# Optimization experiments

Hardware: AMD Instinct MI355X
Metric: run time of the kernel (lower is better)

Reference implementation:

```python
import jax, jax.numpy as jnp
import numpy as np

SHAPES = ((100, 100), (50, 50), (25, 25))  # (H_l, W_l) per level
D, HEADS, HD, L, P = 256, 8, 32, 3, 4


def setup_inputs() -> dict:
    key = jax.random.key(0)
    ks = jax.random.split(key, 12)
    B = 2
    Nq = sum(h * w for h, w in SHAPES)  # 13125
    inp = {
        "query": jax.random.normal(ks[0], (B, Nq, D), jnp.float32),
        "reference_points": jax.random.uniform(ks[1], (B, Nq, L, 2), jnp.float32),
        "value0": jax.random.normal(ks[2], (B, SHAPES[0][0] * SHAPES[0][1], D), jnp.float32),
        "value1": jax.random.normal(ks[3], (B, SHAPES[1][0] * SHAPES[1][1], D), jnp.float32),
        "value2": jax.random.normal(ks[4], (B, SHAPES[2][0] * SHAPES[2][1], D), jnp.float32),
        "W_val": jax.random.normal(ks[5], (D, D), jnp.float32) * 0.05,
        "b_val": jnp.zeros((D,), jnp.float32),
        "W_off": jax.random.normal(ks[6], (D, HEADS * L * P * 2), jnp.float32) * 0.01,
        "b_off": jax.random.normal(ks[7], (HEADS * L * P * 2,), jnp.float32) * 2.0,
        "W_attn": jax.random.normal(ks[8], (D, HEADS * L * P), jnp.float32) * 0.02,
        "b_attn": jnp.zeros((HEADS * L * P,), jnp.float32),
        "W_out": jax.random.normal(ks[9], (D, D), jnp.float32) * 0.05,
        "b_out": jnp.zeros((D,), jnp.float32),
    }
    return inp


def _bilinear_sample(v, Hl, Wl, loc):
    """v: (B, heads, Hl*Wl, hd); loc: (B, Nq, heads, P, 2) normalized coords in [0,1].
    Matches torch F.grid_sample(mode='bilinear', padding_mode='zeros', align_corners=False)
    applied to grid = 2*loc - 1. Returns (B, Nq, heads, P, hd)."""
    B, heads, _, hd = v.shape
    Nq, Pn = loc.shape[1], loc.shape[3]
    # align_corners=False: pixel = ((g+1)*size - 1)/2 with g = 2*loc-1  ->  loc*size - 0.5
    x = loc[..., 0] * Wl - 0.5
    y = loc[..., 1] * Hl - 0.5
    x0 = jnp.floor(x)
    y0 = jnp.floor(y)
    wx1 = x - x0
    wy1 = y - y0
    out = jnp.zeros((B, Nq, heads, Pn, hd), v.dtype)
    for xi, wx in ((x0, 1.0 - wx1), (x0 + 1.0, wx1)):
        for yi, wy in ((y0, 1.0 - wy1), (y0 + 1.0, wy1)):
            inb = (xi >= 0) & (xi < Wl) & (yi >= 0) & (yi < Hl)
            idx = (jnp.clip(yi, 0, Hl - 1) * Wl + jnp.clip(xi, 0, Wl - 1)).astype(jnp.int32)
            idx_t = idx.transpose(0, 2, 1, 3).reshape(B, heads, Nq * Pn)  # (B,H,Nq*P)
            g = jnp.take_along_axis(v, idx_t[..., None], axis=2)  # (B,H,Nq*P,hd)
            g = g.reshape(B, heads, Nq, Pn, hd).transpose(0, 2, 1, 3, 4)
            w = (wx * wy * inb).astype(v.dtype)  # (B,Nq,heads,P)
            out = out + g * w[..., None]
    return out


def _forward(query, reference_points, values, W_val, b_val, W_off, b_off, W_attn, b_attn, W_out, b_out):
    B, Nq, _ = query.shape
    offs = (query @ W_off + b_off).reshape(B, Nq, HEADS, L, P, 2)
    attn = jax.nn.softmax((query @ W_attn + b_attn).reshape(B, Nq, HEADS, L * P), axis=-1)
    attn = attn.reshape(B, Nq, HEADS, L, P)
    out = jnp.zeros((B, Nq, HEADS, HD), query.dtype)
    for lvl, (Hl, Wl) in enumerate(SHAPES):
        # project values, split heads: (B, heads, H*W, hd)
        v = (values[lvl] @ W_val + b_val).reshape(B, Hl * Wl, HEADS, HD).transpose(0, 2, 1, 3)
        norm = jnp.array([Wl, Hl], query.dtype)
        loc = reference_points[:, :, lvl][:, :, None, None, :] + offs[:, :, :, lvl] / norm  # (B,Nq,heads,P,2)
        sampled = _bilinear_sample(v, Hl, Wl, loc)  # (B,Nq,heads,P,hd)
        out = out + jnp.einsum('bnhp,bnhpd->bnhd', attn[:, :, :, lvl], sampled)
    out = out.reshape(B, Nq, D)
    return out @ W_out + b_out  # dropout is identity at eval


def reference(query, reference_points, value0, value1, value2, W_val, b_val, W_off, b_off, W_attn, b_attn, W_out, b_out):
    return _forward(query, reference_points, (value0, value1, value2), W_val, b_val, W_off, b_off, W_attn, b_attn, W_out, b_out)
```

## Files before the change

### kernel.cpp

```cpp
#include <hip/hip_runtime.h>
#include <hip/hip_bf16.h>
#include <math.h>

#define BATCH 2
#define NQ    13125
#define MQ    26250
#define DM    256
#define NH    8
#define HDIM  32
#define NL    3
#define NP    4
#define NTOK  13125

typedef __attribute__((ext_vector_type(8))) short bf16x8;
typedef __attribute__((ext_vector_type(4))) float f32x4;
typedef __attribute__((ext_vector_type(2))) float f32x2;

__device__ __forceinline__ short f2bf(float f) {
    unsigned u = __float_as_uint(f);
    unsigned r = (u + 0x7FFFu + ((u >> 16) & 1u)) >> 16;
    return (short)r;
}
__device__ __forceinline__ float bf2f(unsigned short u) {
    return __uint_as_float((unsigned)u << 16);
}
__device__ __forceinline__ unsigned cvt_pk_bf16(float lo, float hi) {
    unsigned r;
    asm("v_cvt_pk_bf16_f32 %0, %1, %2" : "=v"(r) : "v"(lo), "v"(hi));
    return r;
}

__device__ __forceinline__ void gld_lds16(const short* g, short* l) {
    __builtin_amdgcn_global_load_lds(
        (const __attribute__((address_space(1))) unsigned int*)g,
        (__attribute__((address_space(3))) unsigned int*)l, 16, 0, 0);
}

__global__ __launch_bounds__(256) void wprep_kernel(const float* __restrict__ Wv,
                                                    const float* __restrict__ Wo,
                                                    const float* __restrict__ Wa,
                                                    const float* __restrict__ Wu,
                                                    short* __restrict__ Wt)
{
    const int bid = blockIdx.x;
    const int w  = bid >> 8;
    const int Ns[5]   = {256, 192, 96, 256, 96};
    const int Offs[5] = {0, 65536, 114688, 163840, 139264};
    const int N = Ns[w];
    const int flat = (bid & 255) * 256 + threadIdx.x;
    const int n = flat >> 8, k = flat & 255;
    if (n >= N) return;
    if (w == 4) { Wt[139264 + n * 256 + k] = 0; return; }
    const float* W = (w == 0) ? Wv : ((w == 1) ? Wo : ((w == 2) ? Wa : Wu));
    Wt[Offs[w] + n * 256 + k] = f2bf(W[k * N + n]);
}

__global__ __launch_bounds__(256) void gemm5_kernel(const float* __restrict__ query,
                                                    const float* __restrict__ v0,
                                                    const float* __restrict__ v1,
                                                    const float* __restrict__ v2,
                                                    const short* __restrict__ Wt_val,
                                                    const short* __restrict__ Wt_off,
                                                    const float* __restrict__ b_val,
                                                    const float* __restrict__ b_off,
                                                    const float* __restrict__ b_attn,
                                                    short* __restrict__ vws,
                                                    float* __restrict__ offs,
                                                    float* __restrict__ lgts)
{
    const int e = (blockIdx.x & 7) * 129 + (blockIdx.x >> 3);
    if (e >= 1030) return;
    const int y  = e % 5;
    const int m0 = (e / 5) * 128;

    __shared__ short As[128 * 32];
    __shared__ short Bs[128 * 32];

    const int tid  = threadIdx.x;
    const bool isv = (y < 2);
    const short* Wt = isv ? Wt_val : Wt_off;
    const int n0 = isv ? y * 128 : (y - 2) * 128;

    const int r  = tid >> 1;
    const int h  = tid & 1;
    const int gm = m0 + r;
    const int gmc = (gm < MQ) ? gm : (MQ - 1);
    const float* Arow;
    if (isv) {
        const int b  = gmc / NTOK;
        const int rr = gmc % NTOK;
        if (rr < 10000)      Arow = v0 + (size_t)(b * 10000 + rr) * 256;
        else if (rr < 12500) Arow = v1 + (size_t)(b * 2500 + rr - 10000) * 256;
        else                 Arow = v2 + (size_t)(b * 625 + rr - 12500) * 256;
    } else {
        Arow = query + (size_t)gmc * 256;
    }
    const int pA0 = ((h * 2 + 0) ^ ((r >> 1) & 3)) << 3;
    const int pA1 = ((h * 2 + 1) ^ ((r >> 1) & 3)) << 3;
    short* lAr = As + r * 32;

    const int row0 = tid >> 2;
    const int row1 = row0 + 64;
    const int kqs  = (tid & 3) ^ ((row0 >> 1) & 3);
    const short* gB0 = Wt + (size_t)(n0 + row0) * 256 + kqs * 8;
    const short* gB1 = Wt + (size_t)(n0 + row1) * 256 + kqs * 8;
    short* lB0 = Bs + tid * 8;
    short* lB1 = Bs + (256 + tid) * 8;

    const int lane = tid & 63;
    const int wave = tid >> 6;
    const int wm   = (wave & 1) * 64;
    const int wn   = (wave >> 1) * 64;
    const int ml   = lane & 15;
    const int kq   = lane >> 4;

    f32x4 acc[4][4] = {};

    for (int k0 = 0; k0 < 256; k0 += 32) {
        gld_lds16(gB0 + k0, lB0);
        gld_lds16(gB1 + k0, lB1);

        const float4 a0 = *(const float4*)(Arow + k0 + h * 16 + 0);
        const float4 a1 = *(const float4*)(Arow + k0 + h * 16 + 4);
        const float4 a2 = *(const float4*)(Arow + k0 + h * 16 + 8);
        const float4 a3 = *(const float4*)(Arow + k0 + h * 16 + 12);
        union { bf16x8 v; unsigned u[4]; } t0, t1;
        t0.u[0] = cvt_pk_bf16(a0.x, a0.y); t0.u[1] = cvt_pk_bf16(a0.z, a0.w);
        t0.u[2] = cvt_pk_bf16(a1.x, a1.y); t0.u[3] = cvt_pk_bf16(a1.z, a1.w);
        t1.u[0] = cvt_pk_bf16(a2.x, a2.y); t1.u[1] = cvt_pk_bf16(a2.z, a2.w);
        t1.u[2] = cvt_pk_bf16(a3.x, a3.y); t1.u[3] = cvt_pk_bf16(a3.z, a3.w);
        *(bf16x8*)(lAr + pA0) = t0.v;
        *(bf16x8*)(lAr + pA1) = t1.v;

        __syncthreads();

        bf16x8 af[4], bfr[4];
#pragma unroll
        for (int ti = 0; ti < 4; ++ti) {
            const int rr = wm + ti * 16 + ml;
            af[ti] = *(const bf16x8*)&As[rr * 32 + ((kq ^ ((rr >> 1) & 3)) << 3)];
        }
#pragma unroll
        for (int tj = 0; tj < 4; ++tj) {
            const int rr = wn + tj * 16 + ml;
            bfr[tj] = *(const bf16x8*)&Bs[rr * 32 + ((kq ^ ((rr >> 1) & 3)) << 3)];
        }
#pragma unroll
        for (int ti = 0; ti < 4; ++ti)
#pragma unroll
            for (int tj = 0; tj < 4; ++tj)
                acc[ti][tj] = __builtin_amdgcn_mfma_f32_16x16x32_bf16(af[ti], bfr[tj], acc[ti][tj], 0, 0, 0);

        __syncthreads();
    }

#pragma unroll
    for (int tj = 0; tj < 4; ++tj) {
        const int gn = n0 + wn + tj * 16 + ml;
#pragma unroll
        for (int ti = 0; ti < 4; ++ti) {
#pragma unroll
            for (int rr = 0; rr < 4; ++rr) {
                const int gmo = m0 + wm + ti * 16 + kq * 4 + rr;
                if (gmo >= MQ) continue;
                const float v = acc[ti][tj][rr];
                if (isv) {
                    vws[(size_t)gmo * 256 + gn] = f2bf(v + b_val[gn]);
                } else {
                    if (gn < 192)      offs[(size_t)gmo * 192 + gn]        = v + b_off[gn];
                    else if (gn < 288) lgts[(size_t)gmo * 96 + (gn - 192)] = v + b_attn[gn - 192];
                }
            }
        }
    }
}

__device__ __forceinline__ void gemm_core128(const short* __restrict__ A,
                                             const short* __restrict__ Wt,
                                             int m0, int n0,
                                             f32x4 (&acc)[4][4],
                                             short* As, short* Bs)
{
    const int tid  = threadIdx.x;
    const int lane = tid & 63;
    const int wave = tid >> 6;
    const int wm   = (wave & 1) * 64;
    const int wn   = (wave >> 1) * 64;
    const int ml   = lane & 15;
    const int kq   = lane >> 4;

    const int row0 = tid >> 2;
    const int row1 = row0 + 64;
    const int kqs  = (tid & 3) ^ ((row0 >> 1) & 3);
    const short* gA0 = A  + (size_t)(m0 + row0) * 256 + kqs * 8;
    const short* gA1 = A  + (size_t)(m0 + row1) * 256 + kqs * 8;
    const short* gB0 = Wt + (size_t)(n0 + row0) * 256 + kqs * 8;
    const short* gB1 = Wt + (size_t)(n0 + row1) * 256 + kqs * 8;
    short* lA0 = As + tid * 8;
    short* lA1 = As + (256 + tid) * 8;
    short* lB0 = Bs + tid * 8;
    short* lB1 = Bs + (256 + tid) * 8;
    const bool a0ok = (m0 + row0) < MQ;
    const bool a1ok = (m0 + row1) < MQ;

    for (int k0 = 0; k0 < 256; k0 += 32) {
        if (a0ok) gld_lds16(gA0 + k0, lA0);
        if (a1ok) gld_lds16(gA1 + k0, lA1);
        gld_lds16(gB0 + k0, lB0);
        gld_lds16(gB1 + k0, lB1);
        __syncthreads();

        bf16x8 af[4], bfr[4];
#pragma unroll
        for (int ti = 0; ti < 4; ++ti) {
            const int r = wm + ti * 16 + ml;
            af[ti] = *(const bf16x8*)&As[r * 32 + ((kq ^ ((r >> 1) & 3)) << 3)];
        }
#pragma unroll
        for (int tj = 0; tj < 4; ++tj) {
            const int r = wn + tj * 16 + ml;
            bfr[tj] = *(const bf16x8*)&Bs[r * 32 + ((kq ^ ((r >> 1) & 3)) << 3)];
        }
#pragma unroll
        for (int ti = 0; ti < 4; ++ti)
#pragma unroll
            for (int tj = 0; tj < 4; ++tj)
                acc[ti][tj] = __builtin_amdgcn_mfma_f32_16x16x32_bf16(af[ti], bfr[tj], acc[ti][tj], 0, 0, 0);

        __syncthreads();
    }
}

__global__ __launch_bounds__(256) void ogemm_kernel(const short* __restrict__ A,
                                                    const short* __restrict__ Wt,
                                                    const float* __restrict__ bias,
                                                    float* __restrict__ C)
{
    const int e = (blockIdx.x & 7) * 52 + (blockIdx.x >> 3);
    if (e >= 412) return;
    const int m0 = (e >> 1) * 128;
    const int n0 = (e & 1) * 128;

    __shared__ short As[128 * 32];
    __shared__ short Bs[128 * 32];

    f32x4 acc[4][4] = {};
    gemm_core128(A, Wt, m0, n0, acc, As, Bs);

    const int tid  = threadIdx.x;
    const int lane = tid & 63;
    const int wave = tid >> 6;
    const int wm   = (wave & 1) * 64;
    const int wn   = (wave >> 1) * 64;
    const int ml   = lane & 15;
    const int kq   = lane >> 4;

#pragma unroll
    for (int tj = 0; tj < 4; ++tj) {
        const int gn = n0 + wn + tj * 16 + ml;
#pragma unroll
        for (int ti = 0; ti < 4; ++ti) {
#pragma unroll
            for (int r = 0; r < 4; ++r) {
                const int gm = m0 + wm + ti * 16 + kq * 4 + r;
                if (gm >= MQ) continue;
                C[(size_t)gm * 256 + gn] = acc[ti][tj][r] + bias[gn];
            }
        }
    }
}

__device__ __forceinline__ void pk_acc(f32x2 (&acc)[4], uint4 u, float w) {
    f32x2 w2 = {w, w};
    unsigned ud[4] = {u.x, u.y, u.z, u.w};
#pragma unroll
    for (int d = 0; d < 4; ++d) {
        f32x2 v2;
        v2.x = __uint_as_float(ud[d] << 16);
        v2.y = __uint_as_float(ud[d] & 0xFFFF0000u);
        asm("v_pk_fma_f32 %0, %1, %2, %0" : "+v"(acc[d]) : "v"(v2), "v"(w2));
    }
}

__global__ __launch_bounds__(256) void sample_kernel(const short* __restrict__ vws,
                                                     const float* __restrict__ offs,
                                                     const float* __restrict__ logits,
                                                     const float* __restrict__ refp,
                                                     short* __restrict__ mid)
{
    const int bid = blockIdx.x;
    const int xcd = bid & 7, pos = bid >> 3;
    int g;
    if (xcd < 4) { g = pos * 4 + xcd; }
    else         { g = 1644 + pos * 4 + (xcd - 4); if (g >= 3282) return; }
    const int q0  = g * 8;
    const int tid = threadIdx.x;

    __shared__ float  s_lg[8][96];
    __shared__ float  s_ref[8][6];
    __shared__ float  s_stat[8][NH][2];
    __shared__ float4 s_w[8][96];
    __shared__ int4   s_i[8][96];

    for (int idx = tid; idx < 768; idx += 256) {
        const int qq = idx / 96, s = idx % 96;
        const int q = q0 + qq;
        if (q < MQ) s_lg[qq][s] = logits[(size_t)q * 96 + s];
    }
    if (tid < 48) {
        const int qq = tid / 6, j = tid % 6;
        const int q = q0 + qq;
        if (q < MQ) s_ref[qq][j] = refp[(size_t)q * 6 + j];
    }
    __syncthreads();

    if (tid < 64) {
        const int qq = tid >> 3, h = tid & 7;
        if (q0 + qq < MQ) {
            float mx = -1e30f;
#pragma unroll
            for (int i = 0; i < 12; ++i) mx = fmaxf(mx, s_lg[qq][h * 12 + i]);
            float ssum = 0.f;
#pragma unroll
            for (int i = 0; i < 12; ++i) ssum += __expf(s_lg[qq][h * 12 + i] - mx);
            s_stat[qq][h][0] = mx;
            s_stat[qq][h][1] = 1.f / ssum;
        }
    }
    __syncthreads();

    for (int idx = tid; idx < 768; idx += 256) {
        const int qq = idx / 96, slot = idx % 96;
        const int q  = q0 + qq;
        if (q >= MQ) continue;
        const int b  = q / NQ;
        const int h  = slot & 7, i = slot >> 3;
        const int l  = i >> 2, p = i & 3;

        const int Hs[3] = {100, 50, 25};
        const int Wz[3] = {100, 50, 25};
        const int Lo[3] = {0, 10000, 12500};
        const int Wl = Wz[l], Hl = Hs[l];
        const float fW = (float)Wl, fH = (float)Hl;

        const float aw = __expf(s_lg[qq][h * 12 + i] - s_stat[qq][h][0]) * s_stat[qq][h][1];

        const int oi = (((h * NL) + l) * NP + p) * 2;
        const float2 offp = *(const float2*)(offs + (size_t)q * 192 + oi);
        const float rx = s_ref[qq][l * 2 + 0];
        const float ry = s_ref[qq][l * 2 + 1];

        const float x = (rx + offp.x / fW) * fW - 0.5f;
        const float y = (ry + offp.y / fH) * fH - 0.5f;
        const float x0f = floorf(x), y0f = floorf(y);
        const int   x0 = (int)x0f,  y0 = (int)y0f;
        const float wx1 = x - x0f, wy1 = y - y0f;
        const float wx0 = 1.f - wx1, wy0 = 1.f - wy1;

        const bool xin0 = (x0 >= 0) && (x0 < Wl);
        const bool xin1 = (x0 + 1 >= 0) && (x0 + 1 < Wl);
        const bool yin0 = (y0 >= 0) && (y0 < Hl);
        const bool yin1 = (y0 + 1 >= 0) && (y0 + 1 < Hl);

        const int cx0 = min(max(x0, 0), Wl - 1);
        const int cx1 = min(max(x0 + 1, 0), Wl - 1);
        const int cy0 = min(max(y0, 0), Hl - 1);
        const int cy1 = min(max(y0 + 1, 0), Hl - 1);

        const int base = b * NTOK + Lo[l];
        int4 idxv;
        idxv.x = (base + cy0 * Wl + cx0) << 8;
        idxv.y = (base + cy0 * Wl + cx1) << 8;
        idxv.z = (base + cy1 * Wl + cx0) << 8;
        idxv.w = (base + cy1 * Wl + cx1) << 8;

        float4 w;
        w.x = (xin0 && yin0) ? aw * wx0 * wy0 : 0.f;
        w.y = (xin1 && yin0) ? aw * wx1 * wy0 : 0.f;
        w.z = (xin0 && yin1) ? aw * wx0 * wy1 : 0.f;
        w.w = (xin1 && yin1) ? aw * wx1 * wy1 : 0.f;

        s_w[qq][slot] = w;
        s_i[qq][slot] = idxv;
    }
    __syncthreads();

    {
        const int qq = tid >> 5;
        const int q  = q0 + qq;
        if (q < MQ) {
            const int r   = tid & 31;
            const int h   = r >> 2;
            const int chb = h * HDIM + (r & 3) * 8;
            const short* base = vws + chb;

            float4 w_ = s_w[qq][h];
            int4  id_ = s_i[qq][h];
            uint4 a_ = *(const uint4*)(base + id_.x);
            uint4 b_ = *(const uint4*)(base + id_.y);
            uint4 c_ = *(const uint4*)(base + id_.z);
            uint4 d_ = *(const uint4*)(base + id_.w);

            f32x2 acc[4] = {};
#pragma unroll
            for (int s = 0; s < 12; ++s) {
                const float4 w = w_;
                const uint4 ua = a_, ub = b_, uc = c_, ud = d_;
                if (s < 11) {
                    const int slot = (s + 1) * 8 + h;
                    w_  = s_w[qq][slot];
                    id_ = s_i[qq][slot];
                    a_ = *(const uint4*)(base + id_.x);
                    b_ = *(const uint4*)(base + id_.y);
                    c_ = *(const uint4*)(base + id_.z);
                    d_ = *(const uint4*)(base + id_.w);
                }
                pk_acc(acc, ua, w.x);
                pk_acc(acc, ub, w.y);
                pk_acc(acc, uc, w.z);
                pk_acc(acc, ud, w.w);
            }
            uint4 o;
            o.x = cvt_pk_bf16(acc[0].x, acc[0].y);
            o.y = cvt_pk_bf16(acc[1].x, acc[1].y);
            o.z = cvt_pk_bf16(acc[2].x, acc[2].y);
            o.w = cvt_pk_bf16(acc[3].x, acc[3].y);
            *(uint4*)(mid + (size_t)q * DM + chb) = o;
        }
    }
}

extern "C" void kernel_launch(void* const* d_in, const int* in_sizes, int n_in,
                              void* d_out, int out_size, void* d_ws, size_t ws_size,
                              hipStream_t stream)
{
    const float* query  = (const float*)d_in[0];
    const float* refp   = (const float*)d_in[1];
    const float* v0     = (const float*)d_in[2];
    const float* v1     = (const float*)d_in[3];
    const float* v2     = (const float*)d_in[4];
    const float* W_val  = (const float*)d_in[5];
    const float* b_val  = (const float*)d_in[6];
    const float* W_off  = (const float*)d_in[7];
    const float* b_off  = (const float*)d_in[8];
    const float* W_attn = (const float*)d_in[9];
    const float* b_attn = (const float*)d_in[10];
    const float* W_out  = (const float*)d_in[11];
    const float* b_out  = (const float*)d_in[12];
    float* out = (float*)d_out;

    float* ws   = (float*)d_ws;
    float* offs = ws;
    float* lgts = offs + (size_t)MQ * 192;
    short* vws  = (short*)(lgts + (size_t)MQ * 96);
    short* mid  = vws + (size_t)MQ * DM;
    short* Wt   = mid + (size_t)MQ * DM;
    short* Wt_val = Wt;
    short* Wt_off = Wt + 65536;
    short* Wt_out = Wt + 163840;

    wprep_kernel<<<1280, 256, 0, stream>>>(W_val, W_off, W_attn, W_out, Wt);
    gemm5_kernel<<<1032, 256, 0, stream>>>(query, v0, v1, v2, Wt_val, Wt_off,
                                           b_val, b_off, b_attn, vws, offs, lgts);
    sample_kernel<<<3288, 256, 0, stream>>>(vws, offs, lgts, refp, mid);
    ogemm_kernel<<<416, 256, 0, stream>>>(mid, Wt_out, b_out, out);
}
```

Measured before the change: 227.6 us.

## Fuse output projection GEMM into sampling kernel via LDS-staged tile

The separate output-projection GEMM kernel is removed. Each sampling block now writes its 8 query rows of sampled features as bf16 into a swizzled shared-memory tile, padded to 16 rows with zeros. It then multiplies that tile by W_out with MFMA, adds the bias, and writes the final output directly. This removes the round trip of the intermediate buffer through global memory and one kernel launch. In exchange, half of each 16-row MFMA tile is wasted on padding, and W_out is re-read from global or L2 by every block without LDS staging.

```diff
diff --git a/kernel.cpp b/kernel.cpp
--- a/kernel.cpp
+++ b/kernel.cpp
@@ -175,101 +175,6 @@
     }
 }
 
-__device__ __forceinline__ void gemm_core128(const short* __restrict__ A,
-                                             const short* __restrict__ Wt,
-                                             int m0, int n0,
-                                             f32x4 (&acc)[4][4],
-                                             short* As, short* Bs)
-{
-    const int tid  = threadIdx.x;
-    const int lane = tid & 63;
-    const int wave = tid >> 6;
-    const int wm   = (wave & 1) * 64;
-    const int wn   = (wave >> 1) * 64;
-    const int ml   = lane & 15;
-    const int kq   = lane >> 4;
-
-    const int row0 = tid >> 2;
-    const int row1 = row0 + 64;
-    const int kqs  = (tid & 3) ^ ((row0 >> 1) & 3);
-    const short* gA0 = A  + (size_t)(m0 + row0) * 256 + kqs * 8;
-    const short* gA1 = A  + (size_t)(m0 + row1) * 256 + kqs * 8;
-    const short* gB0 = Wt + (size_t)(n0 + row0) * 256 + kqs * 8;
-    const short* gB1 = Wt + (size_t)(n0 + row1) * 256 + kqs * 8;
-    short* lA0 = As + tid * 8;
-    short* lA1 = As + (256 + tid) * 8;
-    short* lB0 = Bs + tid * 8;
-    short* lB1 = Bs + (256 + tid) * 8;
-    const bool a0ok = (m0 + row0) < MQ;
-    const bool a1ok = (m0 + row1) < MQ;
-
-    for (int k0 = 0; k0 < 256; k0 += 32) {
-        if (a0ok) gld_lds16(gA0 + k0, lA0);
-        if (a1ok) gld_lds16(gA1 + k0, lA1);
-        gld_lds16(gB0 + k0, lB0);
-        gld_lds16(gB1 + k0, lB1);
-        __syncthreads();
-
-        bf16x8 af[4], bfr[4];
-#pragma unroll
-        for (int ti = 0; ti < 4; ++ti) {
-            const int r = wm + ti * 16 + ml;
-            af[ti] = *(const bf16x8*)&As[r * 32 + ((kq ^ ((r >> 1) & 3)) << 3)];
-        }
-#pragma unroll
-        for (int tj = 0; tj < 4; ++tj) {
-            const int r = wn + tj * 16 + ml;
-            bfr[tj] = *(const bf16x8*)&Bs[r * 32 + ((kq ^ ((r >> 1) & 3)) << 3)];
-        }
-#pragma unroll
-        for (int ti = 0; ti < 4; ++ti)
-#pragma unroll
-            for (int tj = 0; tj < 4; ++tj)
-                acc[ti][tj] = __builtin_amdgcn_mfma_f32_16x16x32_bf16(af[ti], bfr[tj], acc[ti][tj], 0, 0, 0);
-
-        __syncthreads();
-    }
-}
-
-__global__ __launch_bounds__(256) void ogemm_kernel(const short* __restrict__ A,
-                                                    const short* __restrict__ Wt,
-                                                    const float* __restrict__ bias,
-                                                    float* __restrict__ C)
-{
-    const int e = (blockIdx.x & 7) * 52 + (blockIdx.x >> 3);
-    if (e >= 412) return;
-    const int m0 = (e >> 1) * 128;
-    const int n0 = (e & 1) * 128;
-
-    __shared__ short As[128 * 32];
-    __shared__ short Bs[128 * 32];
-
-    f32x4 acc[4][4] = {};
-    gemm_core128(A, Wt, m0, n0, acc, As, Bs);
-
-    const int tid  = threadIdx.x;
-    const int lane = tid & 63;
-    const int wave = tid >> 6;
-    const int wm   = (wave & 1) * 64;
-    const int wn   = (wave >> 1) * 64;
-    const int ml   = lane & 15;
-    const int kq   = lane >> 4;
-
-#pragma unroll
-    for (int tj = 0; tj < 4; ++tj) {
-        const int gn = n0 + wn + tj * 16 + ml;
-#pragma unroll
-        for (int ti = 0; ti < 4; ++ti) {
-#pragma unroll
-            for (int r = 0; r < 4; ++r) {
-                const int gm = m0 + wm + ti * 16 + kq * 4 + r;
-                if (gm >= MQ) continue;
-                C[(size_t)gm * 256 + gn] = acc[ti][tj][r] + bias[gn];
-            }
-        }
-    }
-}
-
 __device__ __forceinline__ void pk_acc(f32x2 (&acc)[4], uint4 u, float w) {
     f32x2 w2 = {w, w};
     unsigned ud[4] = {u.x, u.y, u.z, u.w};
@@ -286,13 +191,16 @@
                                                      const float* __restrict__ offs,
                                                      const float* __restrict__ logits,
                                                      const float* __restrict__ refp,
-                                                     short* __restrict__ mid)
+                                                     const short* __restrict__ Wt_out,
+                                                     const float* __restrict__ b_out,
+                                                     float* __restrict__ out)
 {
     const int bid = blockIdx.x;
     const int xcd = bid & 7, pos = bid >> 3;
     int g;
+    bool alive = true;
     if (xcd < 4) { g = pos * 4 + xcd; }
-    else         { g = 1644 + pos * 4 + (xcd - 4); if (g >= 3282) return; }
+    else         { g = 1644 + pos * 4 + (xcd - 4); if (g >= 3282) { g = 0; alive = false; } }
     const int q0  = g * 8;
     const int tid = threadIdx.x;
 
@@ -301,6 +209,14 @@
     __shared__ float  s_stat[8][NH][2];
     __shared__ float4 s_w[8][96];
     __shared__ int4   s_i[8][96];
+    __shared__ short  s_mid[16][256];
+
+    if (!alive) return;
+
+    {
+        short z[8] = {0,0,0,0,0,0,0,0};
+        *(bf16x8*)&s_mid[8 + (tid >> 5)][(tid & 31) * 8] = *(bf16x8*)z;
+    }
 
     for (int idx = tid; idx < 768; idx += 256) {
         const int qq = idx / 96, s = idx % 96;
@@ -388,10 +304,10 @@
     {
         const int qq = tid >> 5;
         const int q  = q0 + qq;
+        const int r   = tid & 31;
+        const int h   = r >> 2;
+        const int chb = h * HDIM + (r & 3) * 8;
         if (q < MQ) {
-            const int r   = tid & 31;
-            const int h   = r >> 2;
-            const int chb = h * HDIM + (r & 3) * 8;
             const short* base = vws + chb;
 
             float4 w_ = s_w[qq][h];
@@ -420,12 +336,53 @@
                 pk_acc(acc, uc, w.z);
                 pk_acc(acc, ud, w.w);
             }
-            uint4 o;
-            o.x = cvt_pk_bf16(acc[0].x, acc[0].y);
-            o.y = cvt_pk_bf16(acc[1].x, acc[1].y);
-            o.z = cvt_pk_bf16(acc[2].x, acc[2].y);
-            o.w = cvt_pk_bf16(acc[3].x, acc[3].y);
-            *(uint4*)(mid + (size_t)q * DM + chb) = o;
+            union { bf16x8 v; unsigned u[4]; } o;
+            o.u[0] = cvt_pk_bf16(acc[0].x, acc[0].y);
+            o.u[1] = cvt_pk_bf16(acc[1].x, acc[1].y);
+            o.u[2] = cvt_pk_bf16(acc[2].x, acc[2].y);
+            o.u[3] = cvt_pk_bf16(acc[3].x, acc[3].y);
+            const int gran = (chb >> 3) ^ (qq & 7);
+            *(bf16x8*)&s_mid[qq][gran * 8] = o.v;
+        } else {
+            short z[8] = {0,0,0,0,0,0,0,0};
+            const int gran = (chb >> 3);
+            *(bf16x8*)&s_mid[qq][gran * 8] = *(bf16x8*)z;
+        }
+    }
+    __syncthreads();
+
+    {
+        const int lane = tid & 63;
+        const int wv   = tid >> 6;
+        const int n0w  = wv * 64;
+        const int ml   = lane & 15;
+        const int kq   = lane >> 4;
+
+        f32x4 oacc[4] = {};
+#pragma unroll
+        for (int kc = 0; kc < 8; ++kc) {
+            const int gran = ((kc * 4 + kq) ^ (ml & 7)) * 8;
+            const bf16x8 af = *(const bf16x8*)&s_mid[ml][gran];
+#pragma unroll
+            for (int ti = 0; ti < 4; ++ti) {
+                const int n = n0w + ti * 16 + ml;
+                const bf16x8 bfr = *(const bf16x8*)(Wt_out + (size_t)n * 256 + kc * 32 + kq * 8);
+                oacc[ti] = __builtin_amdgcn_mfma_f32_16x16x32_bf16(af, bfr, oacc[ti], 0, 0, 0);
+            }
+        }
+
+#pragma unroll
+        for (int ti = 0; ti < 4; ++ti) {
+            const int n = n0w + ti * 16 + ml;
+            const float bb = b_out[n];
+#pragma unroll
+            for (int reg = 0; reg < 4; ++reg) {
+                const int qrow = kq * 4 + reg;
+                if (qrow < 8) {
+                    const int q = q0 + qrow;
+                    if (q < MQ) out[(size_t)q * 256 + n] = oacc[ti][reg] + bb;
+                }
+            }
         }
     }
 }
@@ -453,8 +410,7 @@
     float* offs = ws;
     float* lgts = offs + (size_t)MQ * 192;
     short* vws  = (short*)(lgts + (size_t)MQ * 96);
-    short* mid  = vws + (size_t)MQ * DM;
-    short* Wt   = mid + (size_t)MQ * DM;
+    short* Wt   = vws + (size_t)MQ * DM;
     short* Wt_val = Wt;
     short* Wt_off = Wt + 65536;
     short* Wt_out = Wt + 163840;
@@ -462,6 +418,5 @@
     wprep_kernel<<<1280, 256, 0, stream>>>(W_val, W_off, W_attn, W_out, Wt);
     gemm5_kernel<<<1032, 256, 0, stream>>>(query, v0, v1, v2, Wt_val, Wt_off,
                                            b_val, b_off, b_attn, vws, offs, lgts);
-    sample_kernel<<<3288, 256, 0, stream>>>(vws, offs, lgts, refp, mid);
-    ogemm_kernel<<<416, 256, 0, stream>>>(mid, Wt_out, b_out, out);
-}
+    sample_kernel<<<3288, 256, 0, stream>>>(vws, offs, lgts, refp, Wt_out, b_out, out);
+}
```

New measurement: 252.9 us. 1.11x slower.

## Fuse weight conversion into GEMM kernels and double-buffer activation tiles

Applied to the files above, without the earlier changes.

Removes the separate weight transpose/convert kernel; each GEMM block now loads its full 128x256 weight panel from fp32, converts it to bf16 and stores it in a swizzled 64KB LDS buffer. The query/value GEMM also double-buffers the A tile so that one sync per k-step is dropped and loads overlap with MFMA work. This saves one kernel launch and the global round trip for the weights. In exchange every block repeats the strided fp32 weight read and conversion, and the larger LDS footprint may lower occupancy.

```diff
diff --git a/kernel.cpp b/kernel.cpp
--- a/kernel.cpp
+++ b/kernel.cpp
@@ -36,31 +36,38 @@
         (__attribute__((address_space(3))) unsigned int*)l, 16, 0, 0);
 }
 
-__global__ __launch_bounds__(256) void wprep_kernel(const float* __restrict__ Wv,
-                                                    const float* __restrict__ Wo,
-                                                    const float* __restrict__ Wa,
-                                                    const float* __restrict__ Wu,
-                                                    short* __restrict__ Wt)
+__device__ __forceinline__ void convert_B_panel(const float* src, int stride, short* Bs, int tid)
 {
-    const int bid = blockIdx.x;
-    const int w  = bid >> 8;
-    const int Ns[5]   = {256, 192, 96, 256, 96};
-    const int Offs[5] = {0, 65536, 114688, 163840, 139264};
-    const int N = Ns[w];
-    const int flat = (bid & 255) * 256 + threadIdx.x;
-    const int n = flat >> 8, k = flat & 255;
-    if (n >= N) return;
-    if (w == 4) { Wt[139264 + n * 256 + k] = 0; return; }
-    const float* W = (w == 0) ? Wv : ((w == 1) ? Wo : ((w == 2) ? Wa : Wu));
-    Wt[Offs[w] + n * 256 + k] = f2bf(W[k * N + n]);
+    const int n  = tid & 127;
+    const int kb = (tid >> 7) * 128;
+#pragma unroll
+    for (int c8 = 0; c8 < 16; ++c8) {
+        const int kg = kb + c8 * 8;
+        union { bf16x8 v; unsigned u[4]; } t;
+        if (src) {
+            float f[8];
+#pragma unroll
+            for (int j = 0; j < 8; ++j) f[j] = src[(size_t)(kg + j) * stride];
+            t.u[0] = cvt_pk_bf16(f[0], f[1]);
+            t.u[1] = cvt_pk_bf16(f[2], f[3]);
+            t.u[2] = cvt_pk_bf16(f[4], f[5]);
+            t.u[3] = cvt_pk_bf16(f[6], f[7]);
+        } else {
+            t.u[0] = 0; t.u[1] = 0; t.u[2] = 0; t.u[3] = 0;
+        }
+        const int gg = kg >> 3;
+        const int eg = gg ^ (n & 31);
+        *(bf16x8*)&Bs[n * 256 + eg * 8] = t.v;
+    }
 }
 
 __global__ __launch_bounds__(256) void gemm5_kernel(const float* __restrict__ query,
                                                     const float* __restrict__ v0,
                                                     const float* __restrict__ v1,
                                                     const float* __restrict__ v2,
-                                                    const short* __restrict__ Wt_val,
-                                                    const short* __restrict__ Wt_off,
+                                                    const float* __restrict__ W_val,
+                                                    const float* __restrict__ W_off,
+                                                    const float* __restrict__ W_attn,
                                                     const float* __restrict__ b_val,
                                                     const float* __restrict__ b_off,
                                                     const float* __restrict__ b_attn,
@@ -73,13 +80,26 @@
     const int y  = e % 5;
     const int m0 = (e / 5) * 128;
 
-    __shared__ short As[128 * 32];
-    __shared__ short Bs[128 * 32];
+    __shared__ short Bs[128 * 256];
+    __shared__ short As[2][128 * 32];
 
     const int tid  = threadIdx.x;
     const bool isv = (y < 2);
-    const short* Wt = isv ? Wt_val : Wt_off;
     const int n0 = isv ? y * 128 : (y - 2) * 128;
+
+    {
+        const float* src = nullptr;
+        int stride = 0;
+        const int nl = tid & 127;
+        if (isv) {
+            src = W_val + (y * 128 + nl); stride = 256;
+        } else {
+            const int gn = (y - 2) * 128 + nl;
+            if (gn < 192)      { src = W_off + gn;          stride = 192; }
+            else if (gn < 288) { src = W_attn + (gn - 192); stride = 96;  }
+        }
+        convert_B_panel(src, stride, Bs, tid);
+    }
 
     const int r  = tid >> 1;
     const int h  = tid & 1;
@@ -97,15 +117,6 @@
     }
     const int pA0 = ((h * 2 + 0) ^ ((r >> 1) & 3)) << 3;
     const int pA1 = ((h * 2 + 1) ^ ((r >> 1) & 3)) << 3;
-    short* lAr = As + r * 32;
-
-    const int row0 = tid >> 2;
-    const int row1 = row0 + 64;
-    const int kqs  = (tid & 3) ^ ((row0 >> 1) & 3);
-    const short* gB0 = Wt + (size_t)(n0 + row0) * 256 + kqs * 8;
-    const short* gB1 = Wt + (size_t)(n0 + row1) * 256 + kqs * 8;
-    short* lB0 = Bs + tid * 8;
-    short* lB1 = Bs + (256 + tid) * 8;
 
     const int lane = tid & 63;
     const int wave = tid >> 6;
@@ -114,36 +125,40 @@
     const int ml   = lane & 15;
     const int kq   = lane >> 4;
 
+#define STAGE_A(K0, DST) do {                                                   \
+        const float4 a0 = *(const float4*)(Arow + (K0) + h * 16 + 0);           \
+        const float4 a1 = *(const float4*)(Arow + (K0) + h * 16 + 4);           \
+        const float4 a2 = *(const float4*)(Arow + (K0) + h * 16 + 8);           \
+        const float4 a3 = *(const float4*)(Arow + (K0) + h * 16 + 12);          \
+        union { bf16x8 v; unsigned u[4]; } t0, t1;                              \
+        t0.u[0] = cvt_pk_bf16(a0.x, a0.y); t0.u[1] = cvt_pk_bf16(a0.z, a0.w);   \
+        t0.u[2] = cvt_pk_bf16(a1.x, a1.y); t0.u[3] = cvt_pk_bf16(a1.z, a1.w);   \
+        t1.u[0] = cvt_pk_bf16(a2.x, a2.y); t1.u[1] = cvt_pk_bf16(a2.z, a2.w);   \
+        t1.u[2] = cvt_pk_bf16(a3.x, a3.y); t1.u[3] = cvt_pk_bf16(a3.z, a3.w);   \
+        *(bf16x8*)((DST) + r * 32 + pA0) = t0.v;                                \
+        *(bf16x8*)((DST) + r * 32 + pA1) = t1.v;                                \
+    } while (0)
+
     f32x4 acc[4][4] = {};
 
+    STAGE_A(0, As[0]);
+    __syncthreads();
+
     for (int k0 = 0; k0 < 256; k0 += 32) {
-        gld_lds16(gB0 + k0, lB0);
-        gld_lds16(gB1 + k0, lB1);
-
-        const float4 a0 = *(const float4*)(Arow + k0 + h * 16 + 0);
-        const float4 a1 = *(const float4*)(Arow + k0 + h * 16 + 4);
-        const float4 a2 = *(const float4*)(Arow + k0 + h * 16 + 8);
-        const float4 a3 = *(const float4*)(Arow + k0 + h * 16 + 12);
-        union { bf16x8 v; unsigned u[4]; } t0, t1;
-        t0.u[0] = cvt_pk_bf16(a0.x, a0.y); t0.u[1] = cvt_pk_bf16(a0.z, a0.w);
-        t0.u[2] = cvt_pk_bf16(a1.x, a1.y); t0.u[3] = cvt_pk_bf16(a1.z, a1.w);
-        t1.u[0] = cvt_pk_bf16(a2.x, a2.y); t1.u[1] = cvt_pk_bf16(a2.z, a2.w);
-        t1.u[2] = cvt_pk_bf16(a3.x, a3.y); t1.u[3] = cvt_pk_bf16(a3.z, a3.w);
-        *(bf16x8*)(lAr + pA0) = t0.v;
-        *(bf16x8*)(lAr + pA1) = t1.v;
-
-        __syncthreads();
+        const int cur = (k0 >> 5) & 1;
+        if (k0 < 224) STAGE_A(k0 + 32, As[cur ^ 1]);
 
         bf16x8 af[4], bfr[4];
 #pragma unroll
         for (int ti = 0; ti < 4; ++ti) {
             const int rr = wm + ti * 16 + ml;
-            af[ti] = *(const bf16x8*)&As[rr * 32 + ((kq ^ ((rr >> 1) & 3)) << 3)];
+            af[ti] = *(const bf16x8*)&As[cur][rr * 32 + ((kq ^ ((rr >> 1) & 3)) << 3)];
         }
 #pragma unroll
         for (int tj = 0; tj < 4; ++tj) {
             const int rr = wn + tj * 16 + ml;
-            bfr[tj] = *(const bf16x8*)&Bs[rr * 32 + ((kq ^ ((rr >> 1) & 3)) << 3)];
+            const int eg = (((k0 >> 3) + kq) ^ (rr & 31));
+            bfr[tj] = *(const bf16x8*)&Bs[rr * 256 + eg * 8];
         }
 #pragma unroll
         for (int ti = 0; ti < 4; ++ti)
@@ -153,6 +168,7 @@
 
         __syncthreads();
     }
+#undef STAGE_A
 
 #pragma unroll
     for (int tj = 0; tj < 4; ++tj) {
@@ -175,64 +191,8 @@
     }
 }
 
-__device__ __forceinline__ void gemm_core128(const short* __restrict__ A,
-                                             const short* __restrict__ Wt,
-                                             int m0, int n0,
-                                             f32x4 (&acc)[4][4],
-                                             short* As, short* Bs)
-{
-    const int tid  = threadIdx.x;
-    const int lane = tid & 63;
-    const int wave = tid >> 6;
-    const int wm   = (wave & 1) * 64;
-    const int wn   = (wave >> 1) * 64;
-    const int ml   = lane & 15;
-    const int kq   = lane >> 4;
-
-    const int row0 = tid >> 2;
-    const int row1 = row0 + 64;
-    const int kqs  = (tid & 3) ^ ((row0 >> 1) & 3);
-    const short* gA0 = A  + (size_t)(m0 + row0) * 256 + kqs * 8;
-    const short* gA1 = A  + (size_t)(m0 + row1) * 256 + kqs * 8;
-    const short* gB0 = Wt + (size_t)(n0 + row0) * 256 + kqs * 8;
-    const short* gB1 = Wt + (size_t)(n0 + row1) * 256 + kqs * 8;
-    short* lA0 = As + tid * 8;
-    short* lA1 = As + (256 + tid) * 8;
-    short* lB0 = Bs + tid * 8;
-    short* lB1 = Bs + (256 + tid) * 8;
-    const bool a0ok = (m0 + row0) < MQ;
-    const bool a1ok = (m0 + row1) < MQ;
-
-    for (int k0 = 0; k0 < 256; k0 += 32) {
-        if (a0ok) gld_lds16(gA0 + k0, lA0);
-        if (a1ok) gld_lds16(gA1 + k0, lA1);
-        gld_lds16(gB0 + k0, lB0);
-        gld_lds16(gB1 + k0, lB1);
-        __syncthreads();
-
-        bf16x8 af[4], bfr[4];
-#pragma unroll
-        for (int ti = 0; ti < 4; ++ti) {
-            const int r = wm + ti * 16 + ml;
-            af[ti] = *(const bf16x8*)&As[r * 32 + ((kq ^ ((r >> 1) & 3)) << 3)];
-        }
-#pragma unroll
-        for (int tj = 0; tj < 4; ++tj) {
-            const int r = wn + tj * 16 + ml;
-            bfr[tj] = *(const bf16x8*)&Bs[r * 32 + ((kq ^ ((r >> 1) & 3)) << 3)];
-        }
-#pragma unroll
-        for (int ti = 0; ti < 4; ++ti)
-#pragma unroll
-            for (int tj = 0; tj < 4; ++tj)
-                acc[ti][tj] = __builtin_amdgcn_mfma_f32_16x16x32_bf16(af[ti], bfr[tj], acc[ti][tj], 0, 0, 0);
-
-        __syncthreads();
-    }
-}
-
 __global__ __launch_bounds__(256) void ogemm_kernel(const short* __restrict__ A,
-                                                    const short* __restrict__ Wt,
+                                                    const float* __restrict__ W_out,
                                                     const float* __restrict__ bias,
                                                     float* __restrict__ C)
 {
@@ -241,13 +201,13 @@
     const int m0 = (e >> 1) * 128;
     const int n0 = (e & 1) * 128;
 
+    __shared__ short Bs[128 * 256];
     __shared__ short As[128 * 32];
-    __shared__ short Bs[128 * 32];
-
-    f32x4 acc[4][4] = {};
-    gemm_core128(A, Wt, m0, n0, acc, As, Bs);
 
     const int tid  = threadIdx.x;
+
+    convert_B_panel(W_out + (n0 + (tid & 127)), 256, Bs, tid);
+
     const int lane = tid & 63;
     const int wave = tid >> 6;
     const int wm   = (wave & 1) * 64;
@@ -255,16 +215,55 @@
     const int ml   = lane & 15;
     const int kq   = lane >> 4;
 
+    const int row0 = tid >> 2;
+    const int row1 = row0 + 64;
+    const int kqs  = (tid & 3) ^ ((row0 >> 1) & 3);
+    const short* gA0 = A + (size_t)(m0 + row0) * 256 + kqs * 8;
+    const short* gA1 = A + (size_t)(m0 + row1) * 256 + kqs * 8;
+    short* lA0 = As + tid * 8;
+    short* lA1 = As + (256 + tid) * 8;
+    const bool a0ok = (m0 + row0) < MQ;
+    const bool a1ok = (m0 + row1) < MQ;
+
+    f32x4 acc[4][4] = {};
+
+    for (int k0 = 0; k0 < 256; k0 += 32) {
+        if (a0ok) gld_lds16(gA0 + k0, lA0);
+        if (a1ok) gld_lds16(gA1 + k0, lA1);
+        __syncthreads();
+
+        bf16x8 af[4], bfr[4];
+#pragma unroll
+        for (int ti = 0; ti < 4; ++ti) {
+            const int r = wm + ti * 16 + ml;
+            af[ti] = *(const bf16x8*)&As[r * 32 + ((kq ^ ((r >> 1) & 3)) << 3)];
+        }
+#pragma unroll
+        for (int tj = 0; tj < 4; ++tj) {
+            const int r = wn + tj * 16 + ml;
+            const int eg = (((k0 >> 3) + kq) ^ (r & 31));
+            bfr[tj] = *(const bf16x8*)&Bs[r * 256 + eg * 8];
+        }
+#pragma unroll
+        for (int ti = 0; ti < 4; ++ti)
+#pragma unroll
+            for (int tj = 0; tj < 4; ++tj)
+                acc[ti][tj] = __builtin_amdgcn_mfma_f32_16x16x32_bf16(af[ti], bfr[tj], acc[ti][tj], 0, 0, 0);
+
+        __syncthreads();
+    }
+
 #pragma unroll
     for (int tj = 0; tj < 4; ++tj) {
         const int gn = n0 + wn + tj * 16 + ml;
+        const float bb = bias[gn];
 #pragma unroll
         for (int ti = 0; ti < 4; ++ti) {
 #pragma unroll
             for (int r = 0; r < 4; ++r) {
                 const int gm = m0 + wm + ti * 16 + kq * 4 + r;
                 if (gm >= MQ) continue;
-                C[(size_t)gm * 256 + gn] = acc[ti][tj][r] + bias[gn];
+                C[(size_t)gm * 256 + gn] = acc[ti][tj][r] + bb;
             }
         }
     }
@@ -454,14 +453,9 @@
     float* lgts = offs + (size_t)MQ * 192;
     short* vws  = (short*)(lgts + (size_t)MQ * 96);
     short* mid  = vws + (size_t)MQ * DM;
-    short* Wt   = mid + (size_t)MQ * DM;
-    short* Wt_val = Wt;
-    short* Wt_off = Wt + 65536;
-    short* Wt_out = Wt + 163840;
-
-    wprep_kernel<<<1280, 256, 0, stream>>>(W_val, W_off, W_attn, W_out, Wt);
-    gemm5_kernel<<<1032, 256, 0, stream>>>(query, v0, v1, v2, Wt_val, Wt_off,
+
+    gemm5_kernel<<<1032, 256, 0, stream>>>(query, v0, v1, v2, W_val, W_off, W_attn,
                                            b_val, b_off, b_attn, vws, offs, lgts);
     sample_kernel<<<3288, 256, 0, stream>>>(vws, offs, lgts, refp, mid);
-    ogemm_kernel<<<416, 256, 0, stream>>>(mid, Wt_out, b_out, out);
-}
+    ogemm_kernel<<<416, 256, 0, stream>>>(mid, W_out, b_out, out);
+}
```

After: 242.3 us. +6.5%, slower.

## Double-buffer LDS tiles in both GEMM kernels to overlap loads with MFMA

Applied to the files above, without the earlier changes.

Both the fused input-projection GEMM and the output-projection GEMM now use two LDS buffers per operand. The next K-slice is prefetched while MFMAs run on the current one, which removes one barrier per iteration. In the fused kernel the fp32-to-bf16 conversion of A is deferred until after the MFMAs so global load latency is hidden. This doubles LDS use per block and raises register pressure, which may lower occupancy. The output kernel also hoists the bias load out of the inner store loop.

```diff
diff --git a/kernel.cpp b/kernel.cpp
--- a/kernel.cpp
+++ b/kernel.cpp
@@ -73,8 +73,8 @@
     const int y  = e % 5;
     const int m0 = (e / 5) * 128;
 
-    __shared__ short As[128 * 32];
-    __shared__ short Bs[128 * 32];
+    __shared__ short As[2][128 * 32];
+    __shared__ short Bs[2][128 * 32];
 
     const int tid  = threadIdx.x;
     const bool isv = (y < 2);
@@ -97,15 +97,12 @@
     }
     const int pA0 = ((h * 2 + 0) ^ ((r >> 1) & 3)) << 3;
     const int pA1 = ((h * 2 + 1) ^ ((r >> 1) & 3)) << 3;
-    short* lAr = As + r * 32;
 
     const int row0 = tid >> 2;
     const int row1 = row0 + 64;
     const int kqs  = (tid & 3) ^ ((row0 >> 1) & 3);
     const short* gB0 = Wt + (size_t)(n0 + row0) * 256 + kqs * 8;
     const short* gB1 = Wt + (size_t)(n0 + row1) * 256 + kqs * 8;
-    short* lB0 = Bs + tid * 8;
-    short* lB1 = Bs + (256 + tid) * 8;
 
     const int lane = tid & 63;
     const int wave = tid >> 6;
@@ -116,34 +113,48 @@
 
     f32x4 acc[4][4] = {};
 
-    for (int k0 = 0; k0 < 256; k0 += 32) {
-        gld_lds16(gB0 + k0, lB0);
-        gld_lds16(gB1 + k0, lB1);
-
-        const float4 a0 = *(const float4*)(Arow + k0 + h * 16 + 0);
-        const float4 a1 = *(const float4*)(Arow + k0 + h * 16 + 4);
-        const float4 a2 = *(const float4*)(Arow + k0 + h * 16 + 8);
-        const float4 a3 = *(const float4*)(Arow + k0 + h * 16 + 12);
+    {
+        gld_lds16(gB0 + 0, Bs[0] + tid * 8);
+        gld_lds16(gB1 + 0, Bs[0] + (256 + tid) * 8);
+        const float4 a0 = *(const float4*)(Arow + h * 16 + 0);
+        const float4 a1 = *(const float4*)(Arow + h * 16 + 4);
+        const float4 a2 = *(const float4*)(Arow + h * 16 + 8);
+        const float4 a3 = *(const float4*)(Arow + h * 16 + 12);
         union { bf16x8 v; unsigned u[4]; } t0, t1;
         t0.u[0] = cvt_pk_bf16(a0.x, a0.y); t0.u[1] = cvt_pk_bf16(a0.z, a0.w);
         t0.u[2] = cvt_pk_bf16(a1.x, a1.y); t0.u[3] = cvt_pk_bf16(a1.z, a1.w);
         t1.u[0] = cvt_pk_bf16(a2.x, a2.y); t1.u[1] = cvt_pk_bf16(a2.z, a2.w);
         t1.u[2] = cvt_pk_bf16(a3.x, a3.y); t1.u[3] = cvt_pk_bf16(a3.z, a3.w);
-        *(bf16x8*)(lAr + pA0) = t0.v;
-        *(bf16x8*)(lAr + pA1) = t1.v;
-
-        __syncthreads();
+        *(bf16x8*)(As[0] + r * 32 + pA0) = t0.v;
+        *(bf16x8*)(As[0] + r * 32 + pA1) = t1.v;
+    }
+    __syncthreads();
+
+#pragma unroll
+    for (int t = 0; t < 8; ++t) {
+        const int cur = t & 1, nxt = cur ^ 1;
+        const int k0  = t * 32;
+
+        float4 a0, a1, a2, a3;
+        if (t < 7) {
+            gld_lds16(gB0 + k0 + 32, Bs[nxt] + tid * 8);
+            gld_lds16(gB1 + k0 + 32, Bs[nxt] + (256 + tid) * 8);
+            a0 = *(const float4*)(Arow + k0 + 32 + h * 16 + 0);
+            a1 = *(const float4*)(Arow + k0 + 32 + h * 16 + 4);
+            a2 = *(const float4*)(Arow + k0 + 32 + h * 16 + 8);
+            a3 = *(const float4*)(Arow + k0 + 32 + h * 16 + 12);
+        }
 
         bf16x8 af[4], bfr[4];
 #pragma unroll
         for (int ti = 0; ti < 4; ++ti) {
             const int rr = wm + ti * 16 + ml;
-            af[ti] = *(const bf16x8*)&As[rr * 32 + ((kq ^ ((rr >> 1) & 3)) << 3)];
+            af[ti] = *(const bf16x8*)&As[cur][rr * 32 + ((kq ^ ((rr >> 1) & 3)) << 3)];
         }
 #pragma unroll
         for (int tj = 0; tj < 4; ++tj) {
             const int rr = wn + tj * 16 + ml;
-            bfr[tj] = *(const bf16x8*)&Bs[rr * 32 + ((kq ^ ((rr >> 1) & 3)) << 3)];
+            bfr[tj] = *(const bf16x8*)&Bs[cur][rr * 32 + ((kq ^ ((rr >> 1) & 3)) << 3)];
         }
 #pragma unroll
         for (int ti = 0; ti < 4; ++ti)
@@ -151,6 +162,15 @@
             for (int tj = 0; tj < 4; ++tj)
                 acc[ti][tj] = __builtin_amdgcn_mfma_f32_16x16x32_bf16(af[ti], bfr[tj], acc[ti][tj], 0, 0, 0);
 
+        if (t < 7) {
+            union { bf16x8 v; unsigned u[4]; } t0, t1;
+            t0.u[0] = cvt_pk_bf16(a0.x, a0.y); t0.u[1] = cvt_pk_bf16(a0.z, a0.w);
+            t0.u[2] = cvt_pk_bf16(a1.x, a1.y); t0.u[3] = cvt_pk_bf16(a1.z, a1.w);
+            t1.u[0] = cvt_pk_bf16(a2.x, a2.y); t1.u[1] = cvt_pk_bf16(a2.z, a2.w);
+            t1.u[2] = cvt_pk_bf16(a3.x, a3.y); t1.u[3] = cvt_pk_bf16(a3.z, a3.w);
+            *(bf16x8*)(As[nxt] + r * 32 + pA0) = t0.v;
+            *(bf16x8*)(As[nxt] + r * 32 + pA1) = t1.v;
+        }
         __syncthreads();
     }
 
@@ -175,62 +195,6 @@
     }
 }
 
-__device__ __forceinline__ void gemm_core128(const short* __restrict__ A,
-                                             const short* __restrict__ Wt,
-                                             int m0, int n0,
-                                             f32x4 (&acc)[4][4],
-                                             short* As, short* Bs)
-{
-    const int tid  = threadIdx.x;
-    const int lane = tid & 63;
-    const int wave = tid >> 6;
-    const int wm   = (wave & 1) * 64;
-    const int wn   = (wave >> 1) * 64;
-    const int ml   = lane & 15;
-    const int kq   = lane >> 4;
-
-    const int row0 = tid >> 2;
-    const int row1 = row0 + 64;
-    const int kqs  = (tid & 3) ^ ((row0 >> 1) & 3);
-    const short* gA0 = A  + (size_t)(m0 + row0) * 256 + kqs * 8;
-    const short* gA1 = A  + (size_t)(m0 + row1) * 256 + kqs * 8;
-    const short* gB0 = Wt + (size_t)(n0 + row0) * 256 + kqs * 8;
-    const short* gB1 = Wt + (size_t)(n0 + row1) * 256 + kqs * 8;
-    short* lA0 = As + tid * 8;
-    short* lA1 = As + (256 + tid) * 8;
-    short* lB0 = Bs + tid * 8;
-    short* lB1 = Bs + (256 + tid) * 8;
-    const bool a0ok = (m0 + row0) < MQ;
-    const bool a1ok = (m0 + row1) < MQ;
-
-    for (int k0 = 0; k0 < 256; k0 += 32) {
-        if (a0ok) gld_lds16(gA0 + k0, lA0);
-        if (a1ok) gld_lds16(gA1 + k0, lA1);
-        gld_lds16(gB0 + k0, lB0);
-        gld_lds16(gB1 + k0, lB1);
-        __syncthreads();
-
-        bf16x8 af[4], bfr[4];
-#pragma unroll
-        for (int ti = 0; ti < 4; ++ti) {
-            const int r = wm + ti * 16 + ml;
-            af[ti] = *(const bf16x8*)&As[r * 32 + ((kq ^ ((r >> 1) & 3)) << 3)];
-        }
-#pragma unroll
-        for (int tj = 0; tj < 4; ++tj) {
-            const int r = wn + tj * 16 + ml;
-            bfr[tj] = *(const bf16x8*)&Bs[r * 32 + ((kq ^ ((r >> 1) & 3)) << 3)];
-        }
-#pragma unroll
-        for (int ti = 0; ti < 4; ++ti)
-#pragma unroll
-            for (int tj = 0; tj < 4; ++tj)
-                acc[ti][tj] = __builtin_amdgcn_mfma_f32_16x16x32_bf16(af[ti], bfr[tj], acc[ti][tj], 0, 0, 0);
-
-        __syncthreads();
-    }
-}
-
 __global__ __launch_bounds__(256) void ogemm_kernel(const short* __restrict__ A,
                                                     const short* __restrict__ Wt,
                                                     const float* __restrict__ bias,
@@ -241,11 +205,8 @@
     const int m0 = (e >> 1) * 128;
     const int n0 = (e & 1) * 128;
 
-    __shared__ short As[128 * 32];
-    __shared__ short Bs[128 * 32];
-
-    f32x4 acc[4][4] = {};
-    gemm_core128(A, Wt, m0, n0, acc, As, Bs);
+    __shared__ short As[2][128 * 32];
+    __shared__ short Bs[2][128 * 32];
 
     const int tid  = threadIdx.x;
     const int lane = tid & 63;
@@ -255,16 +216,67 @@
     const int ml   = lane & 15;
     const int kq   = lane >> 4;
 
+    const int row0 = tid >> 2;
+    const int row1 = row0 + 64;
+    const int kqs  = (tid & 3) ^ ((row0 >> 1) & 3);
+    const short* gA0 = A  + (size_t)(m0 + row0) * 256 + kqs * 8;
+    const short* gA1 = A  + (size_t)(m0 + row1) * 256 + kqs * 8;
+    const short* gB0 = Wt + (size_t)(n0 + row0) * 256 + kqs * 8;
+    const short* gB1 = Wt + (size_t)(n0 + row1) * 256 + kqs * 8;
+    const bool a0ok = (m0 + row0) < MQ;
+    const bool a1ok = (m0 + row1) < MQ;
+
+    f32x4 acc[4][4] = {};
+
+    if (a0ok) gld_lds16(gA0, As[0] + tid * 8);
+    if (a1ok) gld_lds16(gA1, As[0] + (256 + tid) * 8);
+    gld_lds16(gB0, Bs[0] + tid * 8);
+    gld_lds16(gB1, Bs[0] + (256 + tid) * 8);
+    __syncthreads();
+
+#pragma unroll
+    for (int t = 0; t < 8; ++t) {
+        const int cur = t & 1, nxt = cur ^ 1;
+        const int k0  = t * 32;
+
+        if (t < 7) {
+            if (a0ok) gld_lds16(gA0 + k0 + 32, As[nxt] + tid * 8);
+            if (a1ok) gld_lds16(gA1 + k0 + 32, As[nxt] + (256 + tid) * 8);
+            gld_lds16(gB0 + k0 + 32, Bs[nxt] + tid * 8);
+            gld_lds16(gB1 + k0 + 32, Bs[nxt] + (256 + tid) * 8);
+        }
+
+        bf16x8 af[4], bfr[4];
+#pragma unroll
+        for (int ti = 0; ti < 4; ++ti) {
+            const int rr = wm + ti * 16 + ml;
+            af[ti] = *(const bf16x8*)&As[cur][rr * 32 + ((kq ^ ((rr >> 1) & 3)) << 3)];
+        }
+#pragma unroll
+        for (int tj = 0; tj < 4; ++tj) {
+            const int rr = wn + tj * 16 + ml;
+            bfr[tj] = *(const bf16x8*)&Bs[cur][rr * 32 + ((kq ^ ((rr >> 1) & 3)) << 3)];
+        }
+#pragma unroll
+        for (int ti = 0; ti < 4; ++ti)
+#pragma unroll
+            for (int tj = 0; tj < 4; ++tj)
+                acc[ti][tj] = __builtin_amdgcn_mfma_f32_16x16x32_bf16(af[ti], bfr[tj], acc[ti][tj], 0, 0, 0);
+
+        __syncthreads();
+    }
+
 #pragma unroll
     for (int tj = 0; tj < 4; ++tj) {
         const int gn = n0 + wn + tj * 16 + ml;
+        const float bb = bias[gn];
 #pragma unroll
         for (int ti = 0; ti < 4; ++ti) {
 #pragma unroll
             for (int r = 0; r < 4; ++r) {
                 const int gm = m0 + wm + ti * 16 + kq * 4 + r;
                 if (gm >= MQ) continue;
-                C[(size_t)gm * 256 + gn] = acc[ti][tj][r] + bias[gn];
+                C[(size_t)gm * 256 + gn] = acc[ti][tj][r] + bb;
             }
         }
     }
```

Measured after the change: 226.0 us. About the same (-0.7%).
